# Performance work log

Hardware: AMD Instinct MI355X
Metric: run time of the kernel (lower is better)

## Reference

```python
import jax, jax.numpy as jnp
import numpy as np

IN_DIM, HID, OUT, B, MAX_LEN = 164, 512, 1, 1024, 128


def _uni(key, shape, fan_in):
    b = 1.0 / np.sqrt(fan_in)
    return jax.random.uniform(key, shape, jnp.float32, -b, b)


def setup_inputs() -> dict:
    rng = np.random.default_rng(0)
    sizes = rng.integers(1, MAX_LEN, size=B)  # lengths in [1, 127]
    T = int(sizes.sum())  # total ragged tokens (~65k)
    key = jax.random.key(0)
    ks = jax.random.split(key, 16)
    return {
        "segment_sizes": jnp.asarray(sizes, jnp.int32),
        "features": jax.random.normal(ks[0], (T, IN_DIM), jnp.float32),
        # encoder MLP: Linear(in,hid) -> ReLU -> Linear(hid,hid) -> ReLU
        "We0": _uni(ks[1], (HID, IN_DIM), IN_DIM), "be0": _uni(ks[2], (HID,), IN_DIM),
        "We1": _uni(ks[3], (HID, HID), HID),       "be1": _uni(ks[4], (HID,), HID),
        # single-layer LSTM, torch gate order (i, f, g, o)
        "Wih": _uni(ks[5], (4 * HID, HID), HID),   "bih": _uni(ks[6], (4 * HID,), HID),
        "Whh": _uni(ks[7], (4 * HID, HID), HID),   "bhh": _uni(ks[8], (4 * HID,), HID),
        # residual MLPs l0, l1
        "Wl0": _uni(ks[9], (HID, HID), HID),  "bl0": _uni(ks[10], (HID,), HID),
        "Wl1": _uni(ks[11], (HID, HID), HID), "bl1": _uni(ks[12], (HID,), HID),
        # decoder Linear(hid, out)
        "Wd": _uni(ks[13], (OUT, HID), HID), "bd": _uni(ks[14], (OUT,), HID),
    }


def reference(segment_sizes, features, We0, be0, We1, be1,
              Wih, bih, Whh, bhh, Wl0, bl0, Wl1, bl1, Wd, bd):
    T = features.shape[0]
    # segment encoder MLP on ragged tokens
    x = jax.nn.relu(features @ We0.T + be0)
    x = jax.nn.relu(x @ We1.T + be1)  # [T, HID]
    # pad_sequence: scatter ragged tokens into [MAX_LEN, B, HID] (zero padded)
    starts = jnp.cumsum(segment_sizes) - segment_sizes
    seg = jnp.repeat(jnp.arange(B), segment_sizes, total_repeat_length=T)
    pos = jnp.arange(T) - starts[seg]
    padded = jnp.zeros((MAX_LEN, B, HID), x.dtype).at[pos, seg].set(x)

    # LSTM scan; note: original runs the LSTM over padded zeros too and takes
    # h after the full MAX_LEN steps (no packing) -- reproduce that exactly.
    def step(carry, xt):
        h, c = carry
        g = xt @ Wih.T + bih + h @ Whh.T + bhh  # [B, 4H]
        i, f, gg, o = jnp.split(g, 4, axis=-1)
        c = jax.nn.sigmoid(f) * c + jax.nn.sigmoid(i) * jnp.tanh(gg)
        h = jax.nn.sigmoid(o) * jnp.tanh(c)
        return (h, c), None

    zeros = jnp.zeros((B, HID), x.dtype)
    (h, _), _ = jax.lax.scan(step, (zeros, zeros), padded)

    out = h  # norm is Identity
    out = jax.nn.relu(out @ Wl0.T + bl0) + out
    out = jax.nn.relu(out @ Wl1.T + bl1) + out
    out = (out @ Wd.T + bd).squeeze()  # [B]
    return out
```

## Files before the change

### kernel.cpp

```cpp
#include <hip/hip_runtime.h>
#include <hip/hip_bf16.h>

typedef __attribute__((ext_vector_type(8))) short short8;
typedef __attribute__((ext_vector_type(4))) float f32x4;

#define DEV __device__ __forceinline__

DEV short f2bf(float f){ __hip_bfloat16 h = __float2bfloat16(f); return *reinterpret_cast<short*>(&h); }
DEV float bf2f(short s){ __hip_bfloat16 h; *reinterpret_cast<short*>(&h) = s; return __bfloat162float(h); }

DEV float sigm(float x){ return 1.f/(1.f + __expf(-x)); }
DEV float tanh_f(float x){
  float ax = fabsf(x);
  float e = __expf(-2.f*ax);
  float t = (1.f - e)/(1.f + e);
  return copysignf(t, x);
}

DEV short8 llc_ld16(const short* p){
  union { unsigned long long u[2]; short8 v; } r;
  r.u[0] = __hip_atomic_load((const unsigned long long*)p,
                             __ATOMIC_RELAXED, __HIP_MEMORY_SCOPE_AGENT);
  r.u[1] = __hip_atomic_load((const unsigned long long*)(p + 4),
                             __ATOMIC_RELAXED, __HIP_MEMORY_SCOPE_AGENT);
  return r.v;
}


__global__ void k_cvt(const float* __restrict__ in, short* __restrict__ out, long n){
  long i = (long)blockIdx.x*blockDim.x + threadIdx.x;
  long st = (long)gridDim.x*blockDim.x;
  for (; i < n; i += st) out[i] = f2bf(in[i]);
}

__global__ void k_cvt_pad(const float* __restrict__ in, short* __restrict__ out,
                          int rows, int ic, int oc){
  long n = (long)rows*oc;
  long st = (long)gridDim.x*blockDim.x;
  for (long i = (long)blockIdx.x*blockDim.x + threadIdx.x; i < n; i += st){
    int r = (int)(i / oc), c = (int)(i % oc);
    out[i] = (c < ic) ? f2bf(in[(long)r*ic + c]) : (short)0;
  }
}

__global__ void k_bias2(const float* __restrict__ a, const float* __restrict__ b,
                        float* __restrict__ o, int n){
  int i = blockIdx.x*blockDim.x + threadIdx.x;
  if (i < n) o[i] = a[i] + b[i];
}

__global__ void k_scan(const int* __restrict__ sizes, int* __restrict__ starts, int B){
  __shared__ int t[1024];
  int tid = threadIdx.x;
  int v = (tid < B) ? sizes[tid] : 0;
  t[tid] = v;
  __syncthreads();
  for (int off = 1; off < 1024; off <<= 1){
    int add = (tid >= off) ? t[tid-off] : 0;
    __syncthreads();
    t[tid] += add;
    __syncthreads();
  }
  if (tid < B) starts[tid] = t[tid] - v;
}

template<bool RELU, bool RESID, bool OBF, bool OF32, bool AF32>
__global__ __launch_bounds__(256) void k_gemm(
    const void* __restrict__ Araw, int lda, int Ktrue,
    const short* __restrict__ Bw, int ldb,
    const float* __restrict__ bias,
    const float* __restrict__ R,
    short* __restrict__ Cb, float* __restrict__ Cf, int ldc,
    int M, int N, int K)
{
  constexpr int BM = 64, BN = 128, BK = 64;
  __shared__ short lA[(BK/8)*BM*8];
  __shared__ short lB[(BK/8)*BN*8];
  const short* Ab = (const short*)Araw;
  const float* Af = (const float*)Araw;
  const int tid = threadIdx.x;
  const int l = tid & 63, w = tid >> 6;
  const int lr = l & 15, lk = l >> 4;
  const int bm0 = blockIdx.x*BM, bn0 = blockIdx.y*BN;

  f32x4 acc[4][2];
  #pragma unroll
  for (int a = 0; a < 4; a++)
    #pragma unroll
    for (int b = 0; b < 2; b++) acc[a][b] = (f32x4){0.f,0.f,0.f,0.f};

  for (int k0 = 0; k0 < K; k0 += BK){
    #pragma unroll
    for (int i = 0; i < 2; i++){
      int idx = tid + i*256;
      int m = idx >> 3, kc = idx & 7;
      int gm = bm0 + m; if (gm >= M) gm = M-1;
      short8 v;
      if (AF32){
        int kb = k0 + kc*8;
        if (kb + 8 <= Ktrue){
          const float* p = Af + (long)gm*lda + kb;
          float4 f0 = *(const float4*)p;
          float4 f1 = *(const float4*)(p + 4);
          v[0]=f2bf(f0.x); v[1]=f2bf(f0.y); v[2]=f2bf(f0.z); v[3]=f2bf(f0.w);
          v[4]=f2bf(f1.x); v[5]=f2bf(f1.y); v[6]=f2bf(f1.z); v[7]=f2bf(f1.w);
        } else {
          #pragma unroll
          for (int e = 0; e < 8; e++){
            int k = kb + e;
            v[e] = (k < Ktrue) ? f2bf(Af[(long)gm*lda + k]) : (short)0;
          }
        }
      } else {
        v = *(const short8*)(Ab + (long)gm*lda + k0 + kc*8);
      }
      *(short8*)&lA[(kc*BM + m)*8] = v;
    }
    #pragma unroll
    for (int i = 0; i < 4; i++){
      int idx = tid + i*256;
      int n = idx >> 3, kc = idx & 7;
      *(short8*)&lB[(kc*BN + n)*8] = *(const short8*)(Bw + (long)(bn0+n)*ldb + k0 + kc*8);
    }
    __syncthreads();
    #pragma unroll
    for (int kb = 0; kb < 2; kb++){
      short8 af[4], bfv[2];
      #pragma unroll
      for (int mf = 0; mf < 4; mf++)
        af[mf] = *(short8*)&lA[((kb*4+lk)*BM + mf*16 + lr)*8];
      #pragma unroll
      for (int nf = 0; nf < 2; nf++)
        bfv[nf] = *(short8*)&lB[((kb*4+lk)*BN + w*32 + nf*16 + lr)*8];
      #pragma unroll
      for (int mf = 0; mf < 4; mf++)
        #pragma unroll
        for (int nf = 0; nf < 2; nf++)
          acc[mf][nf] = __builtin_amdgcn_mfma_f32_16x16x32_bf16(af[mf], bfv[nf], acc[mf][nf], 0, 0, 0);
    }
    __syncthreads();
  }

  #pragma unroll
  for (int mf = 0; mf < 4; mf++){
    #pragma unroll
    for (int nf = 0; nf < 2; nf++){
      #pragma unroll
      for (int r = 0; r < 4; r++){
        int row = bm0 + mf*16 + lk*4 + r;
        int col = bn0 + w*32 + nf*16 + lr;
        if (row < M){
          float v = acc[mf][nf][r];
          if (bias) v += bias[col];
          if (RELU) v = fmaxf(v, 0.f);
          if (RESID) v += R[(long)row*ldc + col];
          if (OBF) Cb[(long)row*ldc + col] = f2bf(v);
          if (OF32) Cf[(long)row*ldc + col] = v;
        }
      }
    }
  }
}

__global__ __launch_bounds__(256, 1) void k_lstm(
    const short* __restrict__ Whh,
    const short* __restrict__ Wih,
    const short* __restrict__ Xt,
    short* __restrict__ h0, short* __restrict__ h1,
    float* __restrict__ hF,
    const int* __restrict__ sizes, const int* __restrict__ starts,
    const float* __restrict__ bias2, unsigned int* __restrict__ flags)
{
  __shared__ short wx[4*2*16*64*8];
  const int bid = blockIdx.x;
  const int xcd = bid & 7;
  const int q   = bid >> 3;
  const int ht  = q & 15;
  const int bm  = ((q >> 4) << 3) | xcd;
  const int tid = threadIdx.x;
  const int l = tid & 63, wid = tid >> 6;
  const int wr = wid >> 1, wc = wid & 1;
  const int lr = l & 15, lk = l >> 4;
  const int rowbase = bm*64 + wr*32;
  const int j = ht*32 + wc*16 + lr;
  const int fb = bm*16;

  for (int c = tid; c < 8192; c += 256){
    int lane = c & 63;
    int kk  = (c >> 6) & 15;
    int wcs = (c >> 10) & 1;
    int g   = c >> 11;
    int row = g*512 + ht*32 + wcs*16 + (lane & 15);
    int col = kk*32 + (lane >> 4)*8;
    *(short8*)&wx[(size_t)c*8] = *(const short8*)(Wih + (long)row*512 + col);
  }

  short8 Breg[4][16];
  #pragma unroll
  for (int g = 0; g < 4; ++g){
    const short* wp = Whh + (long)(g*512 + j)*512 + lk*8;
    #pragma unroll
    for (int kk = 0; kk < 16; ++kk)
      Breg[g][kk] = *(const short8*)(wp + kk*32);
  }

  float bz[4];
  #pragma unroll
  for (int g = 0; g < 4; ++g) bz[g] = bias2[g*512 + j];

  const int len0 = sizes[rowbase + lr];
  const int len1 = sizes[rowbase + 16 + lr];
  const long xb0 = (long)starts[rowbase + lr]*512;
  const long xb1 = (long)starts[rowbase + 16 + lr]*512;

  __syncthreads();

  float cst[2][4] = {{0.f,0.f,0.f,0.f},{0.f,0.f,0.f,0.f}};
  const short8 z8 = {0,0,0,0,0,0,0,0};
  const int wxw = wc*16*64*8;

  #pragma unroll 1
  for (int t = 0; t < 128; ++t){
    const short* hc = (t & 1) ? h1 : h0;
    short*       hn = (t & 1) ? h0 : h1;
    const bool on0 = t < len0, on1 = t < len1;
    const short* px0 = Xt + xb0 + (on0 ? (long)t*512 : 0) + lk*8;
    const short* px1 = Xt + xb1 + (on1 ? (long)t*512 : 0) + lk*8;

    f32x4 acc[2][4];
    #pragma unroll
    for (int mf = 0; mf < 2; ++mf)
      #pragma unroll
      for (int g = 0; g < 4; ++g) acc[mf][g] = (f32x4){0.f,0.f,0.f,0.f};

    #pragma unroll
    for (int kk = 0; kk < 16; ++kk){
      short8 x0 = on0 ? *(const short8*)(px0 + kk*32) : z8;
      short8 x1 = on1 ? *(const short8*)(px1 + kk*32) : z8;
      #pragma unroll
      for (int g = 0; g < 4; ++g){
        short8 bx = *(short8*)&wx[g*(2*16*64*8) + wxw + (kk*64 + l)*8];
        acc[0][g] = __builtin_amdgcn_mfma_f32_16x16x32_bf16(x0, bx, acc[0][g], 0, 0, 0);
        acc[1][g] = __builtin_amdgcn_mfma_f32_16x16x32_bf16(x1, bx, acc[1][g], 0, 0, 0);
      }
    }

    if (t > 0){
      if (wid == 0){
        const unsigned int want = (unsigned int)t;
        while (true){
          unsigned int v = __hip_atomic_load(&flags[fb + (l & 15)],
                                             __ATOMIC_RELAXED, __HIP_MEMORY_SCOPE_AGENT);
          if (__all(v >= want)) break;
          __builtin_amdgcn_s_sleep(2);
        }
      }
      __syncthreads();
      asm volatile("" ::: "memory");
      __builtin_amdgcn_sched_barrier(0);

      const short* ph = hc + (long)(rowbase + lr)*512 + lk*8;
      short8 ha0[16], ha1[16];
      #pragma unroll
      for (int kk = 0; kk < 16; ++kk){
        ha0[kk] = llc_ld16(ph + kk*32);
        ha1[kk] = llc_ld16(ph + 16*512 + kk*32);
      }
      #pragma unroll
      for (int kk = 0; kk < 16; ++kk){
        #pragma unroll
        for (int g = 0; g < 4; ++g){
          acc[0][g] = __builtin_amdgcn_mfma_f32_16x16x32_bf16(ha0[kk], Breg[g][kk], acc[0][g], 0, 0, 0);
          acc[1][g] = __builtin_amdgcn_mfma_f32_16x16x32_bf16(ha1[kk], Breg[g][kk], acc[1][g], 0, 0, 0);
        }
      }
    }

    #pragma unroll
    for (int mf = 0; mf < 2; ++mf)
      #pragma unroll
      for (int r = 0; r < 4; ++r){
        int rb = rowbase + mf*16 + lk*4 + r;
        float ip = acc[mf][0][r] + bz[0];
        float fp = acc[mf][1][r] + bz[1];
        float gp = acc[mf][2][r] + bz[2];
        float op = acc[mf][3][r] + bz[3];
        float cn = sigm(fp)*cst[mf][r] + sigm(ip)*tanh_f(gp);
        float hv = sigm(op)*tanh_f(cn);
        cst[mf][r] = cn;
        if (t < 127){
          unsigned int x16 = (unsigned short)f2bf(hv);
          unsigned int par = (unsigned int)__shfl_xor((int)x16, 1, 64);
          if (!(lr & 1)){
            unsigned int wv = x16 | (par << 16);
            __hip_atomic_store((unsigned int*)(hn + (long)rb*512 + (j & ~1)), wv,
                               __ATOMIC_RELAXED, __HIP_MEMORY_SCOPE_AGENT);
          }
        } else {
          hF[(long)rb*512 + j] = hv;
        }
      }

    if (t < 127){
      asm volatile("s_waitcnt vmcnt(0) lgkmcnt(0)" ::: "memory");
      __syncthreads();
      if (tid == 0)
        __hip_atomic_store(&flags[fb + ht], (unsigned int)(t + 1),
                           __ATOMIC_RELAXED, __HIP_MEMORY_SCOPE_AGENT);
    }
  }
}

__global__ __launch_bounds__(256) void k_dec(const float* __restrict__ X,
                                             const float* __restrict__ Wd,
                                             const float* __restrict__ bd,
                                             float* __restrict__ out, int B){
  int w = threadIdx.x >> 6, l = threadIdx.x & 63;
  int row = blockIdx.x*4 + w;
  if (row >= B) return;
  float s = 0.f;
  #pragma unroll
  for (int e = 0; e < 8; e++){
    int j = l + 64*e;
    s += X[(long)row*512 + j]*Wd[j];
  }
  #pragma unroll
  for (int off = 32; off > 0; off >>= 1) s += __shfl_down(s, off);
  if (l == 0) out[row] = s + bd[0];
}


extern "C" void kernel_launch(void* const* d_in, const int* in_sizes, int n_in,
                              void* d_out, int out_size, void* d_ws, size_t ws_size,
                              hipStream_t stream)
{
  const int*   sizes = (const int*)  d_in[0];
  const float* feat  = (const float*)d_in[1];
  const float* We0   = (const float*)d_in[2];
  const float* be0   = (const float*)d_in[3];
  const float* We1   = (const float*)d_in[4];
  const float* be1   = (const float*)d_in[5];
  const float* Wih   = (const float*)d_in[6];
  const float* bih   = (const float*)d_in[7];
  const float* Whh   = (const float*)d_in[8];
  const float* bhh   = (const float*)d_in[9];
  const float* Wl0   = (const float*)d_in[10];
  const float* bl0   = (const float*)d_in[11];
  const float* Wl1   = (const float*)d_in[12];
  const float* bl1   = (const float*)d_in[13];
  const float* Wd    = (const float*)d_in[14];
  const float* bd    = (const float*)d_in[15];

  const int B = in_sizes[0];
  const int T = in_sizes[1] / 164;
  const int HID = 512;

  char* base = (char*)d_ws;
  size_t off = 0;
  auto alloc = [&](size_t bytes)->char*{
    char* p = base + off;
    off = (off + bytes + 255) & ~(size_t)255;
    return p;
  };

  int*          starts = (int*)         alloc((size_t)B*4);
  float*        bias2  = (float*)       alloc(2048*4);
  unsigned int* flags  = (unsigned int*)alloc(256*4);
  short* We0b   = (short*)alloc((size_t)512*192*2);
  short* We1b   = (short*)alloc((size_t)512*512*2);
  short* Wihb   = (short*)alloc((size_t)2048*512*2);
  short* Whhb   = (short*)alloc((size_t)2048*512*2);
  short* Wl0b   = (short*)alloc((size_t)512*512*2);
  short* Wl1b   = (short*)alloc((size_t)512*512*2);
  short* hA     = (short*)alloc((size_t)B*HID*2);
  short* hB     = (short*)alloc((size_t)B*HID*2);
  float* hF     = (float*)alloc((size_t)B*HID*4);
  float* r1     = (float*)alloc((size_t)B*HID*4);
  short* r1b    = (short*)alloc((size_t)B*HID*2);
  float* r2     = (float*)alloc((size_t)B*HID*4);
  short* X0b    = (short*)alloc((size_t)T*512*2);
  short* Xb     = (short*)alloc((size_t)T*512*2);
  (void)ws_size; (void)n_in; (void)out_size;

  hipMemsetAsync(flags, 0, 256*4, stream);

  k_scan<<<1, 1024, 0, stream>>>(sizes, starts, B);
  k_bias2<<<8, 256, 0, stream>>>(bih, bhh, bias2, 2048);

  auto grd = [](long n){ long g = (n + 255)/256; return (int)(g > 4096 ? 4096 : g); };
  k_cvt_pad<<<grd(512l*192), 256, 0, stream>>>(We0, We0b, 512, 164, 192);
  k_cvt<<<grd(512l*512), 256, 0, stream>>>(We1, We1b, 512l*512);
  k_cvt<<<grd(2048l*512), 256, 0, stream>>>(Wih, Wihb, 2048l*512);
  k_cvt<<<grd(2048l*512), 256, 0, stream>>>(Whh, Whhb, 2048l*512);
  k_cvt<<<grd(512l*512), 256, 0, stream>>>(Wl0, Wl0b, 512l*512);
  k_cvt<<<grd(512l*512), 256, 0, stream>>>(Wl1, Wl1b, 512l*512);

  int mt = (T + 63)/64;
  k_gemm<true,false,true,false,true><<<dim3(mt, 4), 256, 0, stream>>>(
      (const void*)feat, 164, 164, We0b, 192, be0, nullptr, X0b, nullptr, 512, T, 512, 192);
  k_gemm<true,false,true,false,false><<<dim3(mt, 4), 256, 0, stream>>>(
      (const void*)X0b, 512, 512, We1b, 512, be1, nullptr, Xb, nullptr, 512, T, 512, 512);

  k_lstm<<<256, 256, 0, stream>>>(Whhb, Wihb, Xb, hA, hB, hF,
                                  sizes, starts, bias2, flags);

  k_gemm<true,true,true,true,true><<<dim3(16, 4), 256, 0, stream>>>(
      (const void*)hF, 512, 512, Wl0b, 512, bl0, hF, r1b, r1, 512, B, 512, 512);
  k_gemm<true,true,false,true,false><<<dim3(16, 4), 256, 0, stream>>>(
      (const void*)r1b, 512, 512, Wl1b, 512, bl1, r1, nullptr, r2, 512, B, 512, 512);

  k_dec<<<B/4, 256, 0, stream>>>(r2, Wd, bd, (float*)d_out, B);
}
```

Baseline: 2.301 ms.

## Co-locate LSTM batch-tile workgroups per XCD and use L2-scoped h exchange

```diff
diff --git a/kernel.cpp b/kernel.cpp
--- a/kernel.cpp
+++ b/kernel.cpp
@@ -3,6 +3,7 @@
 
 typedef __attribute__((ext_vector_type(8))) short short8;
 typedef __attribute__((ext_vector_type(4))) float f32x4;
+typedef __attribute__((ext_vector_type(4))) int   int4v;
 
 #define DEV __device__ __forceinline__
 
@@ -24,6 +25,18 @@
   r.u[1] = __hip_atomic_load((const unsigned long long*)(p + 4),
                              __ATOMIC_RELAXED, __HIP_MEMORY_SCOPE_AGENT);
   return r.v;
+}
+
+DEV short8 ld16_sc0(const short* p){
+  int4v r;
+  asm volatile("global_load_dwordx4 %0, %1, off sc0" : "=v"(r) : "v"(p));
+  return __builtin_bit_cast(short8, r);
+}
+DEV unsigned ld32_sc0(const unsigned* p){
+  unsigned r;
+  asm volatile("global_load_dword %0, %1, off sc0\n\ts_waitcnt vmcnt(0)"
+               : "=v"(r) : "v"(p) : "memory");
+  return r;
 }
 
 
@@ -166,17 +179,18 @@
     const short* __restrict__ Whh,
     const short* __restrict__ Wih,
     const short* __restrict__ Xt,
-    short* __restrict__ h0, short* __restrict__ h1,
+    short* __restrict__ hR,
     float* __restrict__ hF,
     const int* __restrict__ sizes, const int* __restrict__ starts,
-    const float* __restrict__ bias2, unsigned int* __restrict__ flags)
+    const float* __restrict__ bias2,
+    unsigned int* __restrict__ flags,
+    unsigned int* __restrict__ xcc_tab,
+    unsigned int* __restrict__ done)
 {
   __shared__ short wx[4*2*16*64*8];
   const int bid = blockIdx.x;
-  const int xcd = bid & 7;
-  const int q   = bid >> 3;
-  const int ht  = q & 15;
-  const int bm  = ((q >> 4) << 3) | xcd;
+  const int bm  = ((bid & 7) << 1) | ((bid >> 3) & 1);
+  const int ht  = bid >> 4;
   const int tid = threadIdx.x;
   const int l = tid & 63, wid = tid >> 6;
   const int wr = wid >> 1, wc = wid & 1;
@@ -213,6 +227,29 @@
   const long xb0 = (long)starts[rowbase + lr]*512;
   const long xb1 = (long)starts[rowbase + 16 + lr]*512;
 
+  int xcc;
+  asm volatile("s_getreg_b32 %0, hwreg(HW_REG_XCC_ID)" : "=s"(xcc));
+  if (tid == 0){
+    __hip_atomic_store(&xcc_tab[bid], (unsigned)(xcc + 1),
+                       __ATOMIC_RELAXED, __HIP_MEMORY_SCOPE_AGENT);
+    __hip_atomic_fetch_add(&done[bm], 1u,
+                           __ATOMIC_RELEASE, __HIP_MEMORY_SCOPE_AGENT);
+    while (__hip_atomic_load(&done[bm], __ATOMIC_ACQUIRE,
+                             __HIP_MEMORY_SCOPE_AGENT) < 16u)
+      __builtin_amdgcn_s_sleep(2);
+  }
+  __syncthreads();
+  bool fast = true;
+  {
+    unsigned mine = (unsigned)(xcc + 1);
+    #pragma unroll 1
+    for (int i = 0; i < 16; ++i){
+      int obid = (i << 4) | ((bm & 1) << 3) | (bm >> 1);
+      unsigned v = __hip_atomic_load(&xcc_tab[obid],
+                                     __ATOMIC_RELAXED, __HIP_MEMORY_SCOPE_AGENT);
+      if (v != mine) fast = false;
+    }
+  }
   __syncthreads();
 
   float cst[2][4] = {{0.f,0.f,0.f,0.f},{0.f,0.f,0.f,0.f}};
@@ -221,8 +258,8 @@
 
   #pragma unroll 1
   for (int t = 0; t < 128; ++t){
-    const short* hc = (t & 1) ? h1 : h0;
-    short*       hn = (t & 1) ? h0 : h1;
+    const short* hc = hR + ((size_t)((t + 7) & 7) << 19);
+    short*       hn = hR + ((size_t)(t & 7) << 19);
     const bool on0 = t < len0, on1 = t < len1;
     const short* px0 = Xt + xb0 + (on0 ? (long)t*512 : 0) + lk*8;
     const short* px1 = Xt + xb1 + (on1 ? (long)t*512 : 0) + lk*8;
@@ -247,12 +284,20 @@
 
     if (t > 0){
       if (wid == 0){
-        const unsigned int want = (unsigned int)t;
-        while (true){
-          unsigned int v = __hip_atomic_load(&flags[fb + (l & 15)],
-                                             __ATOMIC_RELAXED, __HIP_MEMORY_SCOPE_AGENT);
-          if (__all(v >= want)) break;
-          __builtin_amdgcn_s_sleep(2);
+        const unsigned want = (unsigned)t;
+        if (fast){
+          while (true){
+            unsigned v = ld32_sc0(&flags[fb + (l & 15)]);
+            if (__all(v >= want)) break;
+            __builtin_amdgcn_s_sleep(2);
+          }
+        } else {
+          while (true){
+            unsigned v = __hip_atomic_load(&flags[fb + (l & 15)],
+                                           __ATOMIC_RELAXED, __HIP_MEMORY_SCOPE_AGENT);
+            if (__all(v >= want)) break;
+            __builtin_amdgcn_s_sleep(2);
+          }
         }
       }
       __syncthreads();
@@ -261,10 +306,20 @@
 
       const short* ph = hc + (long)(rowbase + lr)*512 + lk*8;
       short8 ha0[16], ha1[16];
-      #pragma unroll
-      for (int kk = 0; kk < 16; ++kk){
-        ha0[kk] = llc_ld16(ph + kk*32);
-        ha1[kk] = llc_ld16(ph + 16*512 + kk*32);
+      if (fast){
+        #pragma unroll
+        for (int kk = 0; kk < 16; ++kk){
+          ha0[kk] = ld16_sc0(ph + kk*32);
+          ha1[kk] = ld16_sc0(ph + 16*512 + kk*32);
+        }
+        asm volatile("s_waitcnt vmcnt(0)" ::: "memory");
+        __builtin_amdgcn_sched_barrier(0);
+      } else {
+        #pragma unroll
+        for (int kk = 0; kk < 16; ++kk){
+          ha0[kk] = llc_ld16(ph + kk*32);
+          ha1[kk] = llc_ld16(ph + 16*512 + kk*32);
+        }
       }
       #pragma unroll
       for (int kk = 0; kk < 16; ++kk){
@@ -289,12 +344,13 @@
         float hv = sigm(op)*tanh_f(cn);
         cst[mf][r] = cn;
         if (t < 127){
-          unsigned int x16 = (unsigned short)f2bf(hv);
-          unsigned int par = (unsigned int)__shfl_xor((int)x16, 1, 64);
+          unsigned x16 = (unsigned short)f2bf(hv);
+          unsigned par = (unsigned)__shfl_xor((int)x16, 1, 64);
           if (!(lr & 1)){
-            unsigned int wv = x16 | (par << 16);
-            __hip_atomic_store((unsigned int*)(hn + (long)rb*512 + (j & ~1)), wv,
-                               __ATOMIC_RELAXED, __HIP_MEMORY_SCOPE_AGENT);
+            unsigned wv = x16 | (par << 16);
+            unsigned* dst = (unsigned*)(hn + (long)rb*512 + (j & ~1));
+            if (fast) *(volatile unsigned*)dst = wv;
+            else __hip_atomic_store(dst, wv, __ATOMIC_RELAXED, __HIP_MEMORY_SCOPE_AGENT);
           }
         } else {
           hF[(long)rb*512 + j] = hv;
@@ -304,9 +360,11 @@
     if (t < 127){
       asm volatile("s_waitcnt vmcnt(0) lgkmcnt(0)" ::: "memory");
       __syncthreads();
-      if (tid == 0)
-        __hip_atomic_store(&flags[fb + ht], (unsigned int)(t + 1),
-                           __ATOMIC_RELAXED, __HIP_MEMORY_SCOPE_AGENT);
+      if (tid == 0){
+        if (fast) *(volatile unsigned*)&flags[fb + ht] = (unsigned)(t + 1);
+        else __hip_atomic_store(&flags[fb + ht], (unsigned)(t + 1),
+                                __ATOMIC_RELAXED, __HIP_MEMORY_SCOPE_AGENT);
+      }
     }
   }
 }
@@ -365,24 +423,26 @@
 
   int*          starts = (int*)         alloc((size_t)B*4);
   float*        bias2  = (float*)       alloc(2048*4);
-  unsigned int* flags  = (unsigned int*)alloc(256*4);
+  unsigned int* ctrl   = (unsigned int*)alloc(4096);
+  unsigned int* flags  = ctrl;
+  unsigned int* xcc_tab= ctrl + 256;
+  unsigned int* done   = ctrl + 512;
+  short* hR     = (short*)alloc(((size_t)8) << 20);
   short* We0b   = (short*)alloc((size_t)512*192*2);
   short* We1b   = (short*)alloc((size_t)512*512*2);
   short* Wihb   = (short*)alloc((size_t)2048*512*2);
   short* Whhb   = (short*)alloc((size_t)2048*512*2);
   short* Wl0b   = (short*)alloc((size_t)512*512*2);
   short* Wl1b   = (short*)alloc((size_t)512*512*2);
-  short* hA     = (short*)alloc((size_t)B*HID*2);
-  short* hB     = (short*)alloc((size_t)B*HID*2);
   float* hF     = (float*)alloc((size_t)B*HID*4);
   float* r1     = (float*)alloc((size_t)B*HID*4);
   short* r1b    = (short*)alloc((size_t)B*HID*2);
   float* r2     = (float*)alloc((size_t)B*HID*4);
   short* X0b    = (short*)alloc((size_t)T*512*2);
   short* Xb     = (short*)alloc((size_t)T*512*2);
-  (void)ws_size; (void)n_in; (void)out_size;
-
-  hipMemsetAsync(flags, 0, 256*4, stream);
+  (void)n_in; (void)out_size; (void)ws_size;
+
+  hipMemsetAsync(ctrl, 0, 4096, stream);
 
   k_scan<<<1, 1024, 0, stream>>>(sizes, starts, B);
   k_bias2<<<8, 256, 0, stream>>>(bih, bhh, bias2, 2048);
@@ -401,8 +461,8 @@
   k_gemm<true,false,true,false,false><<<dim3(mt, 4), 256, 0, stream>>>(
       (const void*)X0b, 512, 512, We1b, 512, be1, nullptr, Xb, nullptr, 512, T, 512, 512);
 
-  k_lstm<<<256, 256, 0, stream>>>(Whhb, Wihb, Xb, hA, hB, hF,
-                                  sizes, starts, bias2, flags);
+  k_lstm<<<256, 256, 0, stream>>>(Whhb, Wihb, Xb, hR, hF,
+                                  sizes, starts, bias2, flags, xcc_tab, done);
 
   k_gemm<true,true,true,true,true><<<dim3(16, 4), 256, 0, stream>>>(
       (const void*)hF, 512, 512, Wl0b, 512, bl0, hF, r1b, r1, 512, B, 512, 512);
```

After: 2.283 ms. Within noise of the previous version (-0.8%).
